# Performance work log

Hardware: AMD Instinct MI355X
Metric: run time of the kernel (lower is better)

Reference implementation:

```python
import jax, jax.numpy as jnp
import numpy as np

B, L, E = 512, 50, 512
VOCAB = 32000
EPS = 1e-5


def setup_inputs() -> dict:
    key = jax.random.key(0)
    ks = jax.random.split(key, 16)
    inp = {
        'src_tokens': jax.random.randint(ks[0], (B, L), 0, VOCAB, dtype=jnp.int32),
        'trg_tokens': jax.random.randint(ks[1], (B, L), 0, VOCAB, dtype=jnp.int32),
        'pad_idx': 1,
        'emb_src': jax.random.normal(ks[2], (VOCAB, E), jnp.float32) * 0.02,
        'emb_trg': jax.random.normal(ks[3], (VOCAB, E), jnp.float32) * 0.02,
        'W1': jax.random.normal(ks[4], (20, E), jnp.float32) / np.sqrt(E),  # Conv1d(1,20,k=E) kernel squeezed
        'b1': jax.random.normal(ks[5], (20,), jnp.float32) * 0.01,
        'g1': jnp.ones((20,), jnp.float32),
        'beta1': jnp.zeros((20,), jnp.float32),
        'W2': jax.random.normal(ks[6], (40, 20, 3, 3), jnp.float32) / np.sqrt(20 * 9),
        'b2': jax.random.normal(ks[7], (40,), jnp.float32) * 0.01,
        'g2': jnp.ones((40,), jnp.float32),
        'beta2': jnp.zeros((40,), jnp.float32),
        'Wfc1': jax.random.normal(ks[8], (20, 40 * 11 * 11), jnp.float32) / np.sqrt(40 * 11 * 11),
        'bfc1': jnp.zeros((20,), jnp.float32),
        'Wfc2': jax.random.normal(ks[9], (1, 20), jnp.float32) / np.sqrt(20),
        'bfc2': jnp.zeros((1,), jnp.float32),
    }
    return inp


def _maxpool2(x):  # [B,C,H,W] -> 2x2/2 valid max pool
    return jax.lax.reduce_window(x, -jnp.inf, jax.lax.max, (1, 1, 2, 2), (1, 1, 2, 2), 'VALID')


def reference(src_tokens, trg_tokens, pad_idx, emb_src, emb_trg, W1, b1, g1, beta1,
              W2, b2, g2, beta2, Wfc1, bfc1, Wfc2, bfc2):
    src_e = emb_src[src_tokens]  # [B,L,E]
    trg_e = emb_trg[trg_tokens]  # [B,L,E]

    def conv1_bn_relu(x):
        # per-sample Conv1d(1,20,k=E): collapses E -> scalar per position/channel
        f = jnp.einsum('ble,ce->blc', x, W1) + b1  # [B,L,20]
        # per-sample BatchNorm1d in training mode: stats over the L positions of each sample
        mu = jnp.mean(f, axis=1, keepdims=True)
        var = jnp.var(f, axis=1, keepdims=True)  # biased, as torch uses for normalization
        f = (f - mu) * jax.lax.rsqrt(var + EPS) * g1 + beta1
        return jax.nn.relu(f)

    s = conv1_bn_relu(src_e)  # [B,L,20]
    t = conv1_bn_relu(trg_e)  # [B,L,20]

    # broadcast outer-sum: out[b,i,j,c] = s[b,j,c] + t[b,i,c]
    out = s[:, None, :, :] + t[:, :, None, :]          # [B,L,L,20]
    out = jnp.transpose(out, (0, 3, 1, 2))             # [B,20,L,L]
    out = _maxpool2(out)                                # [B,20,25,25]

    out = jax.lax.conv_general_dilated(out, W2, (1, 1), 'VALID') + b2[None, :, None, None]  # [B,40,23,23]
    # BatchNorm2d training mode: stats over (batch, H, W)
    mu = jnp.mean(out, axis=(0, 2, 3), keepdims=True)
    var = jnp.var(out, axis=(0, 2, 3), keepdims=True)
    out = (out - mu) * jax.lax.rsqrt(var + EPS) * g2[None, :, None, None] + beta2[None, :, None, None]
    out = jax.nn.relu(out)
    out = _maxpool2(out)                                # [B,40,11,11]

    out = out.reshape(out.shape[0], -1)                 # [B,4840]
    out = out @ Wfc1.T + bfc1
    out = out @ Wfc2.T + bfc2
    return jax.nn.sigmoid(out)                          # [B,1]
```

## Files before the change

### kernel.cpp

```cpp
#include <hip/hip_runtime.h>
#include <hip/hip_bf16.h>

#define EPS 1e-5f

__device__ __forceinline__ float bf2f(unsigned short u) {
  union { unsigned int i; float f; } x; x.i = ((unsigned int)u) << 16; return x.f;
}
__device__ __forceinline__ float loadp(const void* p, int i, bool f32) {
  return f32 ? ((const float*)p)[i] : bf2f(((const unsigned short*)p)[i]);
}
__device__ __forceinline__ bool detect_f32(const void* g1) {
  return ((const unsigned int*)g1)[0] == 0x3F800000u;
}

__global__ __launch_bounds__(256) void k0_prep(
    const void* __restrict__ W1, const void* __restrict__ W2,
    const void* __restrict__ Wfc1,
    const void* __restrict__ g1, const void* __restrict__ beta1,
    const void* __restrict__ g2, const void* __restrict__ beta2,
    const void* __restrict__ bfc1, const void* __restrict__ Wfc2,
    const void* __restrict__ bfc2,
    float* __restrict__ W1T, float* __restrict__ WT, float* __restrict__ WS,
    float* __restrict__ Wfc1T, float* __restrict__ prm)
{
  const bool f32 = detect_f32(g1);
  int g = blockIdx.x * 256 + threadIdx.x;
  const int NT = 64 * 256;
  for (int i = g; i < 512 * 20; i += NT) {
    int e = i / 20, c = i - e * 20;
    W1T[i] = loadp(W1, c * 512 + e, f32);
  }
  for (int i = g; i < 40 * 3 * 20; i += NT) {
    int o = i / 60, r = i - o * 60;
    int k = r / 20, c = r - k * 20;
    float st = 0.f, ss = 0.f;
    for (int q = 0; q < 3; ++q) {
      st += loadp(W2, ((o * 20 + c) * 3 + k) * 3 + q, f32);
      ss += loadp(W2, ((o * 20 + c) * 3 + q) * 3 + k, f32);
    }
    WT[(o * 3 + k) * 20 + c] = st;
    WS[(o * 3 + k) * 20 + c] = ss;
  }
  for (int i = g; i < 4840 * 20; i += NT) {
    int kk = i / 4840, idx = i - kk * 4840;
    Wfc1T[idx * 20 + kk] = loadp(Wfc1, i, f32);
  }
  if (g < 20)        prm[g] = loadp(g1,    g,       f32);
  else if (g < 40)   prm[g] = loadp(beta1, g - 20,  f32);
  else if (g < 80)   prm[g] = loadp(g2,    g - 40,  f32);
  else if (g < 120)  prm[g] = loadp(beta2, g - 80,  f32);
  else if (g < 140)  prm[g] = loadp(bfc1,  g - 120, f32);
  else if (g < 160)  prm[g] = loadp(Wfc2,  g - 140, f32);
  else if (g == 160) prm[g] = loadp(bfc2,  0,       f32);
}

__global__ __launch_bounds__(512) void k12_fused(
    const int* __restrict__ src_tok, const int* __restrict__ trg_tok,
    const void* __restrict__ emb_src, const void* __restrict__ emb_trg,
    const void* __restrict__ g1flag,
    const float* __restrict__ W1T,
    const float* __restrict__ WT, const float* __restrict__ WS,
    const float* __restrict__ prm,
    float* __restrict__ C1, float* __restrict__ R, float* __restrict__ S2)
{
  __shared__ float part[8 * 64 * 21];
  __shared__ float fl[1000];
  __shared__ float wl[2400];
  __shared__ float pmax[500];
  __shared__ float convl[40 * 24];
  __shared__ float sc[20], sh[20];
  const bool f32 = detect_f32(g1flag);
  int bb = blockIdx.x;
  int side = bb >> 9, b = bb & 511;
  int t = threadIdx.x;
  int lane = t & 63;
  int ch = __builtin_amdgcn_readfirstlane(t >> 6);

  float acc[20];
#pragma unroll
  for (int c = 0; c < 20; ++c) acc[c] = 0.f;
  if (lane < 50) {
    int tok = side ? trg_tok[b * 50 + lane] : src_tok[b * 50 + lane];
    const void* emb = side ? emb_trg : emb_src;
    if (f32) {
      const float4* rowp = (const float4*)((const float*)emb + (size_t)tok * 512 + ch * 64);
      for (int half = 0; half < 2; ++half) {
        float4 u[8];
#pragma unroll
        for (int q = 0; q < 8; ++q) u[q] = rowp[half * 8 + q];
#pragma unroll
        for (int q = 0; q < 8; ++q) {
          float v[4] = { u[q].x, u[q].y, u[q].z, u[q].w };
          const float* w = W1T + (ch * 64 + half * 32 + q * 4) * 20;
#pragma unroll
          for (int j = 0; j < 4; ++j)
#pragma unroll
            for (int c = 0; c < 20; ++c) acc[c] = fmaf(v[j], w[j * 20 + c], acc[c]);
        }
      }
    } else {
      const uint4* rowp = (const uint4*)((const unsigned short*)emb + (size_t)tok * 512 + ch * 64);
      uint4 u[8];
#pragma unroll
      for (int q = 0; q < 8; ++q) u[q] = rowp[q];
#pragma unroll
      for (int q = 0; q < 8; ++q) {
        const unsigned int* qu = (const unsigned int*)&u[q];
        float v[8];
#pragma unroll
        for (int j = 0; j < 4; ++j) {
          union { unsigned int i; float f; } lo, hi;
          lo.i = qu[j] << 16; hi.i = qu[j] & 0xffff0000u;
          v[2 * j] = lo.f; v[2 * j + 1] = hi.f;
        }
        const float* w = W1T + (ch * 64 + q * 8) * 20;
#pragma unroll
        for (int j = 0; j < 8; ++j)
#pragma unroll
          for (int c = 0; c < 20; ++c) acc[c] = fmaf(v[j], w[j * 20 + c], acc[c]);
      }
    }
    float* pp = &part[(ch * 64 + lane) * 21];
#pragma unroll
    for (int c = 0; c < 20; ++c) pp[c] = acc[c];
  }
  {
    const float* wsrc = side ? WT : WS;
    for (int i = t; i < 2400; i += 512) wl[i] = wsrc[i];
  }
  __syncthreads();
  for (int i = t; i < 1000; i += 512) {
    int l = i / 20, c = i - l * 20;
    float s = 0.f;
#pragma unroll
    for (int c2 = 0; c2 < 8; ++c2) s += part[(c2 * 64 + l) * 21 + c];
    fl[i] = s;
  }
  __syncthreads();
  if (t < 20) {
    float s = 0.f, s2 = 0.f;
#pragma unroll
    for (int l = 0; l < 50; ++l) { float v = fl[l * 20 + t]; s += v; s2 += v * v; }
    float mu = s * (1.0f / 50.0f);
    float var = s2 * (1.0f / 50.0f) - mu * mu;
    float k = prm[t] * rsqrtf(var + EPS);
    sc[t] = k; sh[t] = prm[20 + t] - k * mu;
  }
  __syncthreads();
  for (int i = t; i < 500; i += 512) {
    int p = i / 20, c = i - p * 20;
    float k = sc[c], s0 = sh[c];
    float v0 = fmaxf(k * fl[(2 * p) * 20 + c] + s0, 0.f);
    float v1 = fmaxf(k * fl[(2 * p + 1) * 20 + c] + s0, 0.f);
    pmax[i] = fmaxf(v0, v1);
  }
  __syncthreads();
  for (int i = t; i < 920; i += 512) {
    int o = i / 23, y = i - o * 23;
    float a = 0.f;
#pragma unroll
    for (int ky = 0; ky < 3; ++ky) {
      const float* wr = &wl[(o * 3 + ky) * 20];
      const float* pr = &pmax[(y + ky) * 20];
#pragma unroll
      for (int c = 0; c < 20; ++c) a = fmaf(wr[c], pr[c], a);
    }
    C1[((size_t)o * 1024 + bb) * 23 + y] = a;
    convl[o * 24 + y] = a;
  }
  __syncthreads();
  if (t < 40) {
    float s = 0.f, s2 = 0.f;
#pragma unroll
    for (int y = 0; y < 23; ++y) { float v = convl[t * 24 + y]; s += v; s2 += v * v; }
    R[t * 1024 + bb] = s;
    S2[t * 1024 + bb] = s2;
  }
}

__global__ __launch_bounds__(256) void k3_bn2(
    const float* __restrict__ R, const float* __restrict__ S2,
    const float* __restrict__ prm,
    float* __restrict__ bn2)
{
  int o = blockIdx.x, t = threadIdx.x;
  float s1a = 0, s2a = 0, s1b = 0, s2b = 0, sab = 0;
  for (int b = t; b < 512; b += 256) {
    float ra = R[o * 1024 + 512 + b], rb = R[o * 1024 + b];
    s1a += ra; s1b += rb; sab += ra * rb;
    s2a += S2[o * 1024 + 512 + b];
    s2b += S2[o * 1024 + b];
  }
  __shared__ float Rd[5][256];
  Rd[0][t] = s1a; Rd[1][t] = s2a; Rd[2][t] = s1b; Rd[3][t] = s2b; Rd[4][t] = sab;
  __syncthreads();
  for (int s = 128; s > 0; s >>= 1) {
    if (t < s) {
#pragma unroll
      for (int q = 0; q < 5; ++q) Rd[q][t] += Rd[q][t + s];
    }
    __syncthreads();
  }
  if (t == 0) {
    const float invN = 1.0f / (512.0f * 23.0f);
    float muA = Rd[0][0] * invN, muB = Rd[2][0] * invN;
    float ea2 = Rd[1][0] * invN - muA * muA;
    float eb2 = Rd[3][0] * invN - muB * muB;
    float cross = 2.0f * (Rd[4][0] * (1.0f / (529.0f * 512.0f)) - muA * muB);
    float var = ea2 + eb2 + cross;
    float k = prm[40 + o] * rsqrtf(var + EPS);
    bn2[o] = k;
    bn2[40 + o] = prm[80 + o] - k * (muA + muB);
  }
}

__global__ __launch_bounds__(256) void k4_fc(
    const float* __restrict__ C1,
    const float* __restrict__ bn2,
    const float* __restrict__ Wfc1T,
    const float* __restrict__ prm,
    const void* __restrict__ g1flag,
    void* __restrict__ outv)
{
  const bool f32 = detect_f32(g1flag);
  int b = blockIdx.x, t = threadIdx.x;
  __shared__ float mA[440], mB[440];
  __shared__ float k2s[40], c2s[40];
  __shared__ float red[20][256];
  __shared__ float o1[20];
  if (t < 40) k2s[t] = bn2[t];
  else if (t < 80) c2s[t - 40] = bn2[t];
  __syncthreads();
  for (int i = t; i < 440; i += 256) {
    int o = i / 11, y = i - o * 11;
    const float* pa = C1 + ((size_t)o * 1024 + 512 + b) * 23;
    const float* pb = C1 + ((size_t)o * 1024 + b) * 23;
    float a0 = pa[2 * y], a1 = pa[2 * y + 1];
    float b0 = pb[2 * y], b1 = pb[2 * y + 1];
    if (k2s[o] >= 0.f) { mA[i] = fmaxf(a0, a1); mB[i] = fmaxf(b0, b1); }
    else               { mA[i] = fminf(a0, a1); mB[i] = fminf(b0, b1); }
  }
  __syncthreads();
  float acc[20];
#pragma unroll
  for (int c = 0; c < 20; ++c) acc[c] = 0.f;
  for (int idx = t; idx < 4840; idx += 256) {
    int o = idx / 121, r = idx - o * 121;
    int y = r / 11, x = r - y * 11;
    float p = fmaxf(k2s[o] * (mA[o * 11 + y] + mB[o * 11 + x]) + c2s[o], 0.f);
    const float* w = Wfc1T + idx * 20;
#pragma unroll
    for (int c = 0; c < 20; ++c) acc[c] = fmaf(p, w[c], acc[c]);
  }
#pragma unroll
  for (int c = 0; c < 20; ++c) red[c][t] = acc[c];
  __syncthreads();
  for (int s = 128; s > 0; s >>= 1) {
    if (t < s) {
#pragma unroll
      for (int c = 0; c < 20; ++c) red[c][t] += red[c][t + s];
    }
    __syncthreads();
  }
  if (t < 20) o1[t] = red[t][0] + prm[120 + t];
  __syncthreads();
  if (t == 0) {
    float z = prm[160];
#pragma unroll
    for (int c = 0; c < 20; ++c) z = fmaf(prm[140 + c], o1[c], z);
    float sg = 1.0f / (1.0f + expf(-z));
    if (f32) ((float*)outv)[b] = sg;
    else     ((__hip_bfloat16*)outv)[b] = __float2bfloat16(sg);
  }
}

extern "C" void kernel_launch(void* const* d_in, const int* in_sizes, int n_in,
                              void* d_out, int out_size, void* d_ws, size_t ws_size,
                              hipStream_t stream) {
  const int* src_tok = (const int*)d_in[0];
  const int* trg_tok = (const int*)d_in[1];
  const void* emb_src = d_in[3];
  const void* emb_trg = d_in[4];
  const void* W1    = d_in[5];
  const void* g1    = d_in[7];
  const void* beta1 = d_in[8];
  const void* W2    = d_in[9];
  const void* g2    = d_in[11];
  const void* beta2 = d_in[12];
  const void* Wfc1  = d_in[13];
  const void* bfc1  = d_in[14];
  const void* Wfc2  = d_in[15];
  const void* bfc2  = d_in[16];

  char* ws = (char*)d_ws;
  float* W1T   = (float*)(ws + 0);
  float* WT    = (float*)(ws + 40960);
  float* WS    = (float*)(ws + 50560);
  float* Wfc1T = (float*)(ws + 60160);
  float* prm   = (float*)(ws + 447360);
  float* bn2   = (float*)(ws + 448384);
  float* R     = (float*)(ws + 448896);
  float* S2    = (float*)(ws + 612736);
  float* C1    = (float*)(ws + 776576);

  k0_prep<<<64, 256, 0, stream>>>(W1, W2, Wfc1, g1, beta1, g2, beta2, bfc1, Wfc2,
                                  bfc2, W1T, WT, WS, Wfc1T, prm);
  k12_fused<<<1024, 512, 0, stream>>>(src_tok, trg_tok, emb_src, emb_trg, g1,
                                      W1T, WT, WS, prm, C1, R, S2);
  k3_bn2<<<40, 256, 0, stream>>>(R, S2, prm, bn2);
  k4_fc<<<512, 256, 0, stream>>>(C1, bn2, Wfc1T, prm, g1, d_out);
}
```

Measured before the change: 203.5 us.

## Alias k12 shared buffers to raise occupancy and shuffle-reduce in k4

In k12_fused the partial-sum buffer is shrunk to 50 positions per wave and reused for the conv weights, pooled values and conv outputs. The weight staging load now happens after the partial reduction so the aliasing is safe, and a launch-bounds hint asks for more resident blocks. This cuts LDS per block so more blocks can fit per CU. The cost is that the weight-load latency is no longer hidden behind the partial reduction. k4_fc moves to 512 threads and replaces the 20x256 LDS tree reduction with wave shuffles plus a small cross-wave sum, removing many barriers and much LDS traffic.

```diff
diff --git a/kernel.cpp b/kernel.cpp
--- a/kernel.cpp
+++ b/kernel.cpp
@@ -54,7 +54,7 @@
   else if (g == 160) prm[g] = loadp(bfc2,  0,       f32);
 }
 
-__global__ __launch_bounds__(512) void k12_fused(
+__global__ __launch_bounds__(512, 8) void k12_fused(
     const int* __restrict__ src_tok, const int* __restrict__ trg_tok,
     const void* __restrict__ emb_src, const void* __restrict__ emb_trg,
     const void* __restrict__ g1flag,
@@ -63,12 +63,13 @@
     const float* __restrict__ prm,
     float* __restrict__ C1, float* __restrict__ R, float* __restrict__ S2)
 {
-  __shared__ float part[8 * 64 * 21];
+  __shared__ float partA[8 * 50 * 21];
   __shared__ float fl[1000];
-  __shared__ float wl[2400];
-  __shared__ float pmax[500];
-  __shared__ float convl[40 * 24];
   __shared__ float sc[20], sh[20];
+  float* wl    = partA;
+  float* pmax  = partA + 2400;
+  float* convl = partA + 2900;
+
   const bool f32 = detect_f32(g1flag);
   int bb = blockIdx.x;
   int side = bb >> 9, b = bb & 511;
@@ -120,23 +121,23 @@
           for (int c = 0; c < 20; ++c) acc[c] = fmaf(v[j], w[j * 20 + c], acc[c]);
       }
     }
-    float* pp = &part[(ch * 64 + lane) * 21];
+    float* pp = &partA[(ch * 50 + lane) * 21];
 #pragma unroll
     for (int c = 0; c < 20; ++c) pp[c] = acc[c];
   }
+  __syncthreads();
+  for (int i = t; i < 1000; i += 512) {
+    int l = i / 20, c = i - l * 20;
+    float s = 0.f;
+#pragma unroll
+    for (int c2 = 0; c2 < 8; ++c2) s += partA[(c2 * 50 + l) * 21 + c];
+    fl[i] = s;
+  }
+  __syncthreads();
   {
     const float* wsrc = side ? WT : WS;
     for (int i = t; i < 2400; i += 512) wl[i] = wsrc[i];
   }
-  __syncthreads();
-  for (int i = t; i < 1000; i += 512) {
-    int l = i / 20, c = i - l * 20;
-    float s = 0.f;
-#pragma unroll
-    for (int c2 = 0; c2 < 8; ++c2) s += part[(c2 * 64 + l) * 21 + c];
-    fl[i] = s;
-  }
-  __syncthreads();
   if (t < 20) {
     float s = 0.f, s2 = 0.f;
 #pragma unroll
@@ -214,7 +215,7 @@
   }
 }
 
-__global__ __launch_bounds__(256) void k4_fc(
+__global__ __launch_bounds__(512) void k4_fc(
     const float* __restrict__ C1,
     const float* __restrict__ bn2,
     const float* __restrict__ Wfc1T,
@@ -224,14 +225,15 @@
 {
   const bool f32 = detect_f32(g1flag);
   int b = blockIdx.x, t = threadIdx.x;
+  int lane = t & 63, wv = t >> 6;
   __shared__ float mA[440], mB[440];
   __shared__ float k2s[40], c2s[40];
-  __shared__ float red[20][256];
+  __shared__ float wred[8][20];
   __shared__ float o1[20];
   if (t < 40) k2s[t] = bn2[t];
   else if (t < 80) c2s[t - 40] = bn2[t];
   __syncthreads();
-  for (int i = t; i < 440; i += 256) {
+  for (int i = t; i < 440; i += 512) {
     int o = i / 11, y = i - o * 11;
     const float* pa = C1 + ((size_t)o * 1024 + 512 + b) * 23;
     const float* pb = C1 + ((size_t)o * 1024 + b) * 23;
@@ -244,7 +246,7 @@
   float acc[20];
 #pragma unroll
   for (int c = 0; c < 20; ++c) acc[c] = 0.f;
-  for (int idx = t; idx < 4840; idx += 256) {
+  for (int idx = t; idx < 4840; idx += 512) {
     int o = idx / 121, r = idx - o * 121;
     int y = r / 11, x = r - y * 11;
     float p = fmaxf(k2s[o] * (mA[o * 11 + y] + mB[o * 11 + x]) + c2s[o], 0.f);
@@ -253,16 +255,23 @@
     for (int c = 0; c < 20; ++c) acc[c] = fmaf(p, w[c], acc[c]);
   }
 #pragma unroll
-  for (int c = 0; c < 20; ++c) red[c][t] = acc[c];
-  __syncthreads();
-  for (int s = 128; s > 0; s >>= 1) {
-    if (t < s) {
-#pragma unroll
-      for (int c = 0; c < 20; ++c) red[c][t] += red[c][t + s];
-    }
-    __syncthreads();
-  }
-  if (t < 20) o1[t] = red[t][0] + prm[120 + t];
+  for (int c = 0; c < 20; ++c) {
+    float v = acc[c];
+    v += __shfl_xor(v, 32); v += __shfl_xor(v, 16); v += __shfl_xor(v, 8);
+    v += __shfl_xor(v, 4);  v += __shfl_xor(v, 2);  v += __shfl_xor(v, 1);
+    acc[c] = v;
+  }
+  if (lane == 0) {
+#pragma unroll
+    for (int c = 0; c < 20; ++c) wred[wv][c] = acc[c];
+  }
+  __syncthreads();
+  if (t < 20) {
+    float s = 0.f;
+#pragma unroll
+    for (int q = 0; q < 8; ++q) s += wred[q][t];
+    o1[t] = s + prm[120 + t];
+  }
   __syncthreads();
   if (t == 0) {
     float z = prm[160];
@@ -308,5 +317,5 @@
   k12_fused<<<1024, 512, 0, stream>>>(src_tok, trg_tok, emb_src, emb_trg, g1,
                                       W1T, WT, WS, prm, C1, R, S2);
   k3_bn2<<<40, 256, 0, stream>>>(R, S2, prm, bn2);
-  k4_fc<<<512, 256, 0, stream>>>(C1, bn2, Wfc1T, prm, g1, d_out);
-}
+  k4_fc<<<512, 512, 0, stream>>>(C1, bn2, Wfc1T, prm, g1, d_out);
+}
```

New measurement: 202.9 us. Within noise of the previous version (-0.3%).
